# Kernel optimization log

Measured on AMD Instinct MI355X. Metric: run time of the kernel, lower is better.

Reference implementation:

```python
import jax, jax.numpy as jnp
import numpy as np

G = 512      # number of structures (groups)
CNT = 8192   # residues per structure
S = 8192     # sampled pairs per structure (self.samples)
N = G * CNT  # total residues


def _sample_pairs():
    # Deterministic replication of StochasticRGNLoss.pairs: per-group randint
    # sampling, with group offsets added so indices address the global array.
    rng = np.random.default_rng(0)
    local = rng.integers(0, CNT, size=(G, S, 2))
    # avoid degenerate left==right pairs (zero distance -> NaN grad of norm)
    eq = local[..., 0] == local[..., 1]
    local[..., 1] = np.where(eq, (local[..., 1] + 1) % CNT, local[..., 1])
    offs = (np.arange(G) * CNT)[:, None, None]
    pairs = (local + offs).reshape(-1, 2)
    return pairs[:, 0].astype(np.int32), pairs[:, 1].astype(np.int32)


def setup_inputs() -> dict:
    key = jax.random.key(0)
    k1, k2 = jax.random.split(key)
    inputs = jax.random.normal(k1, (N, 3, 3), dtype=jnp.float32)
    target = jax.random.normal(k2, (N, 3, 3), dtype=jnp.float32)
    left_np, right_np = _sample_pairs()
    return {
        "inputs": inputs,
        "target": target,
        "left": jnp.asarray(left_np),
        "right": jnp.asarray(right_np),
    }


def reference(inputs, target, left, right):
    # take the CA atom (index 1) of each residue frame -> [N, 3]
    ca_in = inputs[:, 1]
    ca_tg = target[:, 1]
    # irregular gather of sampled pairs, pairwise distances -> [P]
    d_in = jnp.linalg.norm(ca_in[left] - ca_in[right], axis=1)
    d_tg = jnp.linalg.norm(ca_tg[left] - ca_tg[right], axis=1)
    return jnp.mean((d_in - d_tg) ** 2)
```

## Files before the change

### kernel.cpp

```cpp
#include <hip/hip_runtime.h>

#define G_GROUPS 512
#define CNT      8192
#define S_PAIRS  8192
#define BLOCK    1024
#define WAVES    (BLOCK / 64)
#define RPW      (CNT / WAVES)
#define CHUNKS   (RPW / 64)
#define PPT      (S_PAIRS / BLOCK)

typedef __attribute__((address_space(3))) void  lds_void;
typedef const __attribute__((address_space(1))) void g_void;

__global__ __launch_bounds__(BLOCK) void rgn_loss_kernel(
    const float* __restrict__ inputs,
    const float* __restrict__ target,
    const int*   __restrict__ left,
    const int*   __restrict__ right,
    float*       __restrict__ out)
{
    __shared__ float4 tab4[CNT];
    __shared__ float  red[WAVES];

    const int tid   = threadIdx.x;
    const int lane  = tid & 63;
    const int wid   = tid >> 6;
    const int g     = blockIdx.x;
    const int gbase = g * CNT;

    const size_t pbase = (size_t)g * S_PAIRS;
    int li[PPT], ri[PPT];
    #pragma unroll
    for (int i = 0; i < PPT; ++i) {
        li[i] = left [pbase + tid + i * BLOCK] - gbase;
        ri[i] = right[pbase + tid + i * BLOCK] - gbase;
    }

    {
        const int rbase = wid * RPW;
        #pragma unroll
        for (int c = 0; c < CHUNKS; ++c) {
            const int r = rbase + c * 64;
            const float* gp = inputs + (size_t)(gbase + r + lane) * 9 + 3;
            __builtin_amdgcn_global_load_lds((g_void*)gp,
                                             (lds_void*)&tab4[r],
                                             16, 0, 0);
        }
    }
    __syncthreads();

    float din[PPT];
    #pragma unroll
    for (int i = 0; i < PPT; ++i) {
        const float4 L = tab4[li[i]];
        const float4 R = tab4[ri[i]];
        const float dx = L.x - R.x;
        const float dy = L.y - R.y;
        const float dz = L.z - R.z;
        din[i] = sqrtf(dx * dx + dy * dy + dz * dz);
    }
    __syncthreads();

    {
        const int rbase = wid * RPW;
        #pragma unroll
        for (int c = 0; c < CHUNKS; ++c) {
            const int r = rbase + c * 64;
            const float* gp = target + (size_t)(gbase + r + lane) * 9 + 3;
            __builtin_amdgcn_global_load_lds((g_void*)gp,
                                             (lds_void*)&tab4[r],
                                             16, 0, 0);
        }
    }
    __syncthreads();

    float acc = 0.0f;
    #pragma unroll
    for (int i = 0; i < PPT; ++i) {
        const float4 L = tab4[li[i]];
        const float4 R = tab4[ri[i]];
        const float dx = L.x - R.x;
        const float dy = L.y - R.y;
        const float dz = L.z - R.z;
        const float d  = din[i] - sqrtf(dx * dx + dy * dy + dz * dz);
        acc += d * d;
    }

    #pragma unroll
    for (int off = 32; off > 0; off >>= 1)
        acc += __shfl_down(acc, off);
    if (lane == 0) red[wid] = acc;
    __syncthreads();
    if (wid == 0) {
        float v = (lane < WAVES) ? red[lane] : 0.0f;
        #pragma unroll
        for (int off = 8; off > 0; off >>= 1)
            v += __shfl_down(v, off);
        if (lane == 0)
            atomicAdd(out, v * (1.0f / ((float)G_GROUPS * (float)S_PAIRS)));
    }
}

extern "C" void kernel_launch(void* const* d_in, const int* in_sizes, int n_in,
                              void* d_out, int out_size, void* d_ws, size_t ws_size,
                              hipStream_t stream) {
    const float* inputs = (const float*)d_in[0];
    const float* target = (const float*)d_in[1];
    const int*   left   = (const int*)d_in[2];
    const int*   right  = (const int*)d_in[3];
    float*       out    = (float*)d_out;

    hipMemsetAsync(out, 0, sizeof(float), stream);
    rgn_loss_kernel<<<G_GROUPS, BLOCK, 0, stream>>>(inputs, target, left, right, out);
}
```

Before: 334.0 us.

## Stream contiguous residue tiles through triple-buffered LDS and compact CA coords

The old code fetched 16 bytes at stride 36 for each residue, which wastes most of each memory transaction. The new code copies the whole contiguous 9-float records in 512-residue tiles into a triple-buffered LDS staging area using async global-to-LDS loads. Threads then extract the CA xyz into a packed 3-float table. Loading of the target tiles is issued before the input distance pass so it overlaps with compute. In exchange the kernel reads the full record bytes, uses more LDS (which may lower occupancy), and adds many barriers plus manual vmcnt waits.

```diff
diff --git a/kernel.cpp b/kernel.cpp
--- a/kernel.cpp
+++ b/kernel.cpp
@@ -5,12 +5,56 @@
 #define S_PAIRS  8192
 #define BLOCK    1024
 #define WAVES    (BLOCK / 64)
-#define RPW      (CNT / WAVES)
-#define CHUNKS   (RPW / 64)
 #define PPT      (S_PAIRS / BLOCK)
+
+#define RAW_DW    (CNT * 9)
+#define TILE_REC  512
+#define TILE_DW   (TILE_REC * 9)
+#define TAB_TILE  (TILE_REC * 3)
+#define NTILES    (CNT / TILE_REC)
+#define NBUF      3
+#define CHUNK_DW  256
+#define NCHUNK    (TILE_DW / CHUNK_DW)
+#define ISSUERS   9
 
 typedef __attribute__((address_space(3))) void  lds_void;
 typedef const __attribute__((address_space(1))) void g_void;
+
+__device__ __forceinline__ void fencebar() {
+    asm volatile("s_waitcnt lgkmcnt(0)" ::: "memory");
+    __builtin_amdgcn_s_barrier();
+    asm volatile("" ::: "memory");
+}
+
+__device__ __forceinline__ void issue_tile(const float* __restrict__ src, int t,
+                                           float* rb, int wid, int lane) {
+    const int c0 = 2 * wid;
+    const float* gp0 = src + (size_t)t * TILE_DW + c0 * CHUNK_DW + lane * 4;
+    __builtin_amdgcn_global_load_lds((g_void*)gp0,
+                                     (lds_void*)(rb + c0 * CHUNK_DW), 16, 0, 0);
+    const float* gp1 = gp0 + CHUNK_DW;
+    __builtin_amdgcn_global_load_lds((g_void*)gp1,
+                                     (lds_void*)(rb + c0 * CHUNK_DW + CHUNK_DW), 16, 0, 0);
+}
+
+#define STAGE_PIPE(SRC)                                                          \
+    _Pragma("unroll")                                                            \
+    for (int t = 0; t < NTILES; ++t) {                                           \
+        if (wid < ISSUERS) {                                                     \
+            if (t < NTILES - 1) asm volatile("s_waitcnt vmcnt(2)" ::: "memory"); \
+            else                asm volatile("s_waitcnt vmcnt(0)" ::: "memory"); \
+        }                                                                        \
+        fencebar();                                                              \
+        {                                                                        \
+            const float* rb = &raw[t % NBUF][0];                                 \
+            float*       tb = &tab[t * TAB_TILE];                                \
+            tb[d0] = rb[rI0];                                                    \
+            if (do2) tb[d1] = rb[rI1];                                           \
+        }                                                                        \
+        if (wid < ISSUERS && t + 2 < NTILES)                                     \
+            issue_tile(SRC, t + 2, &raw[(t + 2) % NBUF][0], wid, lane);          \
+    }                                                                            \
+    fencebar();
 
 __global__ __launch_bounds__(BLOCK) void rgn_loss_kernel(
     const float* __restrict__ inputs,
@@ -19,14 +63,18 @@
     const int*   __restrict__ right,
     float*       __restrict__ out)
 {
-    __shared__ float4 tab4[CNT];
-    __shared__ float  red[WAVES];
+    __shared__ float tab[3 * CNT];
+    __shared__ float raw[NBUF][TILE_DW];
+    __shared__ float red[WAVES];
 
     const int tid   = threadIdx.x;
     const int lane  = tid & 63;
     const int wid   = tid >> 6;
     const int g     = blockIdx.x;
     const int gbase = g * CNT;
+
+    const float* srcA = inputs + (size_t)g * RAW_DW;
+    const float* srcB = target + (size_t)g * RAW_DW;
 
     const size_t pbase = (size_t)g * S_PAIRS;
     int li[PPT], ri[PPT];
@@ -36,52 +84,44 @@
         ri[i] = right[pbase + tid + i * BLOCK] - gbase;
     }
 
-    {
-        const int rbase = wid * RPW;
-        #pragma unroll
-        for (int c = 0; c < CHUNKS; ++c) {
-            const int r = rbase + c * 64;
-            const float* gp = inputs + (size_t)(gbase + r + lane) * 9 + 3;
-            __builtin_amdgcn_global_load_lds((g_void*)gp,
-                                             (lds_void*)&tab4[r],
-                                             16, 0, 0);
-        }
+    const int d0  = tid;
+    const int j0  = d0 / 3;
+    const int rI0 = 9 * j0 + 3 + (d0 - 3 * j0);
+    const int d1  = tid + BLOCK;
+    const int j1  = d1 / 3;
+    const int rI1 = 9 * j1 + 3 + (d1 - 3 * j1);
+    const bool do2 = (tid < TAB_TILE - BLOCK);
+
+    if (wid < ISSUERS) {
+        issue_tile(srcA, 0, &raw[0][0], wid, lane);
+        issue_tile(srcA, 1, &raw[1][0], wid, lane);
     }
-    __syncthreads();
+    STAGE_PIPE(srcA)
+
+    if (wid < ISSUERS) {
+        issue_tile(srcB, 0, &raw[0][0], wid, lane);
+        issue_tile(srcB, 1, &raw[1][0], wid, lane);
+    }
 
     float din[PPT];
     #pragma unroll
     for (int i = 0; i < PPT; ++i) {
-        const float4 L = tab4[li[i]];
-        const float4 R = tab4[ri[i]];
-        const float dx = L.x - R.x;
-        const float dy = L.y - R.y;
-        const float dz = L.z - R.z;
+        const int a = 3 * li[i], b = 3 * ri[i];
+        const float dx = tab[a]     - tab[b];
+        const float dy = tab[a + 1] - tab[b + 1];
+        const float dz = tab[a + 2] - tab[b + 2];
         din[i] = sqrtf(dx * dx + dy * dy + dz * dz);
     }
-    __syncthreads();
 
-    {
-        const int rbase = wid * RPW;
-        #pragma unroll
-        for (int c = 0; c < CHUNKS; ++c) {
-            const int r = rbase + c * 64;
-            const float* gp = target + (size_t)(gbase + r + lane) * 9 + 3;
-            __builtin_amdgcn_global_load_lds((g_void*)gp,
-                                             (lds_void*)&tab4[r],
-                                             16, 0, 0);
-        }
-    }
-    __syncthreads();
+    STAGE_PIPE(srcB)
 
     float acc = 0.0f;
     #pragma unroll
     for (int i = 0; i < PPT; ++i) {
-        const float4 L = tab4[li[i]];
-        const float4 R = tab4[ri[i]];
-        const float dx = L.x - R.x;
-        const float dy = L.y - R.y;
-        const float dz = L.z - R.z;
+        const int a = 3 * li[i], b = 3 * ri[i];
+        const float dx = tab[a]     - tab[b];
+        const float dy = tab[a + 1] - tab[b + 1];
+        const float dz = tab[a + 2] - tab[b + 2];
         const float d  = din[i] - sqrtf(dx * dx + dy * dy + dz * dz);
         acc += d * d;
     }
```

Measured after the change: 332.5 us. No clear change (-0.4%).

## Prefetch target CA coords into registers during input distance phase

Applied to the files above, without the earlier changes.

Replaces the direct global-to-LDS async loads with register-staged loads, so each thread reads its 8 rows into registers and then writes them to LDS. The target rows are now loaded into registers before the first distance pass, so their global latency overlaps the LDS gathers for the input distances, and they are written to LDS after the barrier. This costs extra VGPRs (two float4 arrays of 8) at 1024 threads per block, and it drops the LDS-direct path, which may be less efficient for the 16-byte loads from a 36-byte stride.

```diff
diff --git a/kernel.cpp b/kernel.cpp
--- a/kernel.cpp
+++ b/kernel.cpp
@@ -5,12 +5,8 @@
 #define S_PAIRS  8192
 #define BLOCK    1024
 #define WAVES    (BLOCK / 64)
-#define RPW      (CNT / WAVES)
-#define CHUNKS   (RPW / 64)
 #define PPT      (S_PAIRS / BLOCK)
-
-typedef __attribute__((address_space(3))) void  lds_void;
-typedef const __attribute__((address_space(1))) void g_void;
+#define RPT      (CNT / BLOCK)
 
 __global__ __launch_bounds__(BLOCK) void rgn_loss_kernel(
     const float* __restrict__ inputs,
@@ -36,18 +32,24 @@
         ri[i] = right[pbase + tid + i * BLOCK] - gbase;
     }
 
-    {
-        const int rbase = wid * RPW;
-        #pragma unroll
-        for (int c = 0; c < CHUNKS; ++c) {
-            const int r = rbase + c * 64;
-            const float* gp = inputs + (size_t)(gbase + r + lane) * 9 + 3;
-            __builtin_amdgcn_global_load_lds((g_void*)gp,
-                                             (lds_void*)&tab4[r],
-                                             16, 0, 0);
-        }
+    float4 iv[RPT];
+    #pragma unroll
+    for (int k = 0; k < RPT; ++k) {
+        const float* p = inputs + (size_t)(gbase + tid + k * BLOCK) * 9 + 3;
+        __builtin_memcpy(&iv[k], p, 16);
     }
+    #pragma unroll
+    for (int k = 0; k < RPT; ++k)
+        tab4[tid + k * BLOCK] = iv[k];
     __syncthreads();
+
+    float4 tv[RPT];
+    #pragma unroll
+    for (int k = 0; k < RPT; ++k) {
+        const float* p = target + (size_t)(gbase + tid + k * BLOCK) * 9 + 3;
+        __builtin_memcpy(&tv[k], p, 16);
+    }
+    asm volatile("" ::: "memory");
 
     float din[PPT];
     #pragma unroll
@@ -61,17 +63,9 @@
     }
     __syncthreads();
 
-    {
-        const int rbase = wid * RPW;
-        #pragma unroll
-        for (int c = 0; c < CHUNKS; ++c) {
-            const int r = rbase + c * 64;
-            const float* gp = target + (size_t)(gbase + r + lane) * 9 + 3;
-            __builtin_amdgcn_global_load_lds((g_void*)gp,
-                                             (lds_void*)&tab4[r],
-                                             16, 0, 0);
-        }
-    }
+    #pragma unroll
+    for (int k = 0; k < RPT; ++k)
+        tab4[tid + k * BLOCK] = tv[k];
     __syncthreads();
 
     float acc = 0.0f;
```

After: 348.7 us. +4.4%, slower.
